# Optimization experiments

Hardware: AMD Instinct MI355X
Metric: run time of the kernel (lower is better)

## Reference

```python
import jax, jax.numpy as jnp
import numpy as np

B, T, E, H = 64, 256, 300, 512        # batch, longest_sequence, embed dim, hidden
V, NTAGS, NCLS, DFF = 50000, 17, 18, 256  # vocab, universal POS tags, output classes, dense hidden


def setup_inputs() -> dict:
    key = jax.random.key(0)
    ks = jax.random.split(key, 11)
    su = 1.0 / np.sqrt(H)  # PyTorch LSTMCell/Linear uniform init scale
    return {
        "tokens": jax.random.randint(ks[0], (B, T), 0, V),
        "tags": jax.random.randint(ks[1], (T,), 0, NTAGS),
        "emb": jax.random.normal(ks[2], (V, E), jnp.float32),
        "W_ih": jax.random.uniform(ks[3], (NTAGS, 4 * H, E), jnp.float32, -su, su),
        "W_hh": jax.random.uniform(ks[4], (NTAGS, 4 * H, H), jnp.float32, -su, su),
        "b_ih": jax.random.uniform(ks[5], (NTAGS, 4 * H), jnp.float32, -su, su),
        "b_hh": jax.random.uniform(ks[6], (NTAGS, 4 * H), jnp.float32, -su, su),
        "W1": jax.random.uniform(ks[7], (DFF, H), jnp.float32, -su, su),
        "b1": jax.random.uniform(ks[8], (DFF,), jnp.float32, -su, su),
        "W2": jax.random.uniform(ks[9], (NCLS, DFF), jnp.float32, -1.0 / np.sqrt(DFF), 1.0 / np.sqrt(DFF)),
        "b2": jax.random.uniform(ks[10], (NCLS,), jnp.float32, -1.0 / np.sqrt(DFF), 1.0 / np.sqrt(DFF)),
    }


def reference(tokens, tags, emb, W_ih, W_hh, b_ih, b_hh, W1, b1, W2, b2):
    x = emb[tokens]                     # [B, T, E] embedding lookup
    xs = jnp.swapaxes(x, 0, 1)          # [T, B, E] time-major for scan

    def step(carry, inp):
        h, c = carry
        xt, tag = inp                   # xt: [B, E], tag: scalar int routing the cell
        gates = (xt @ W_ih[tag].T + h @ W_hh[tag].T
                 + b_ih[tag] + b_hh[tag])            # [B, 4H]
        i, f, g, o = jnp.split(gates, 4, axis=-1)    # PyTorch LSTMCell gate order
        i = jax.nn.sigmoid(i)
        f = jax.nn.sigmoid(f)
        g = jnp.tanh(g)
        o = jax.nn.sigmoid(o)
        c = f * c + i * g
        h = o * jnp.tanh(c)
        return (h, c), None

    h0 = jnp.zeros((x.shape[0], H), x.dtype)
    (h, _), _ = jax.lax.scan(step, (h0, h0), (xs, tags))
    # dense head: Linear -> ReLU -> (Dropout inactive at eval) -> Linear
    hid = jax.nn.relu(h @ W1.T + b1)
    return hid @ W2.T + b2              # [B, NCLS] multiclass logits
```

## Files before the change

kernel.cpp:

```cpp
#include <hip/hip_runtime.h>
#include <cstdint>
#include <cstddef>

#define BB   64
#define TT   256
#define EE   300
#define HH   512
#define G4H  2048
#define NCLS 18
#define DFF  256
#define NBLK 256

__device__ __forceinline__ float fast_exp2(float x) { return __builtin_amdgcn_exp2f(x); }
__device__ __forceinline__ float sigmoid_f(float x) {
  return 1.0f / (1.0f + fast_exp2(x * -1.442695040888963f));
}
__device__ __forceinline__ float tanh_f(float x) {
  return 2.0f / (1.0f + fast_exp2(x * -2.885390081777927f)) - 1.0f;
}

__global__ __launch_bounds__(256) void xproj_kernel(
    const int* __restrict__ tokens, const int* __restrict__ tags,
    const float* __restrict__ emb, const float* __restrict__ W_ih,
    const float* __restrict__ b_ih, const float* __restrict__ b_hh,
    float* __restrict__ xW, int t0)
{
  const int tid  = threadIdx.x;
  const int lane = tid & 63;
  const int w    = tid >> 6;
  const int rs   = blockIdx.x & 127;
  const int tl   = blockIdx.x >> 7;
  const int t    = t0 + tl;
  const int tag  = tags[t];
  const int row0 = rs * 16;
  const int kbeg = __builtin_amdgcn_readfirstlane(w * 76);
  const bool full = (w != 3);

  const int tok = tokens[lane * TT + t];
  const float* xrow = emb + (size_t)tok * EE + kbeg;
  float xr[76];
  #pragma unroll
  for (int i = 0; i < 18; ++i) {
    const float4 v = *reinterpret_cast<const float4*>(xrow + i * 4);
    xr[i*4+0] = v.x; xr[i*4+1] = v.y; xr[i*4+2] = v.z; xr[i*4+3] = v.w;
  }
  if (full) {
    const float4 v = *reinterpret_cast<const float4*>(xrow + 72);
    xr[72] = v.x; xr[73] = v.y; xr[74] = v.z; xr[75] = v.w;
  } else {
    xr[72] = 0.f; xr[73] = 0.f; xr[74] = 0.f; xr[75] = 0.f;
  }

  const float* Wbase = W_ih + (size_t)tag * ((size_t)G4H * EE);
  __shared__ float red[4][16][64];
  #pragma unroll
  for (int r = 0; r < 16; ++r) {
    const float* Wr = Wbase + (size_t)(row0 + r) * EE + kbeg;
    float a = 0.f;
    #pragma unroll
    for (int k = 0; k < 72; ++k) a = fmaf(Wr[k], xr[k], a);
    if (full) {
      #pragma unroll
      for (int k = 72; k < 76; ++k) a = fmaf(Wr[k], xr[k], a);
    }
    red[w][r][lane] = a;
  }
  __syncthreads();
  #pragma unroll
  for (int it = 0; it < 4; ++it) {
    const int item = tid + it * 256;
    const int r = item >> 6, b = item & 63;
    const int row = row0 + r;
    float s = red[0][r][b] + red[1][r][b] + red[2][r][b] + red[3][r][b];
    s += b_ih[tag * G4H + row] + b_hh[tag * G4H + row];
    xW[((size_t)tl * G4H + row) * BB + b] = s;
  }
}

__global__ __launch_bounds__(1024) void lstm_seq_kernel(
    const int* __restrict__ tags, const float* __restrict__ W_hh,
    const float* __restrict__ xW, float* __restrict__ hA,
    float* __restrict__ hB, float* __restrict__ cst,
    float* __restrict__ hF, unsigned int* __restrict__ flags,
    int t0, int nsteps)
{
  const int tid  = threadIdx.x;
  const int lane = tid & 63;
  const int w    = tid >> 6;
  const int j0   = blockIdx.x * 2;
  const int kbeg = __builtin_amdgcn_readfirstlane(w * 32);

  __shared__ float red[16][8][64];
  __shared__ float gate[8][64];
  __shared__ float wbuf[2][8][512];

  const int ejj = tid >> 6, eb = tid & 63;
  const size_t eidx = (size_t)(j0 + ejj) * BB + eb;
  float creg = (tid < 128) ? cst[eidx] : 0.f;

  const int rr = tid >> 6, rb = tid & 63;
  const int rrow = j0 + (rr & 1) + (rr >> 1) * HH;
  float xw_cur = 0.f;
  if (tid < 512) xw_cur = xW[((size_t)0 * G4H + rrow) * BB + rb];

  const int pr  = w >> 1;
  const int phb = w & 1;
  const size_t prow_off = (size_t)(j0 + (pr & 1) + (pr >> 1) * HH) * HH
                          + phb * 256 + lane * 4;

  {
    const int tag0 = tags[t0];
    const float4 w0 = *reinterpret_cast<const float4*>(
        W_hh + (size_t)tag0 * ((size_t)G4H * HH) + prow_off);
    *reinterpret_cast<float4*>(&wbuf[0][pr][phb * 256 + lane * 4]) = w0;
  }
  __syncthreads();

  for (int s = 0; s < nsteps; ++s) {
    const int t   = t0 + s;
    const int cur = s & 1;
    const float* h_in  = (t & 1) ? hB : hA;
    float*       h_out = (t & 1) ? hA : hB;

    float xr[32];
    const float* hp0 = h_in + (size_t)kbeg * BB + lane;
    const float* hp1 = hp0 + 16 * BB;
    asm volatile(
      "global_load_dword %0,  %32, off sc0 sc1\n\t"
      "global_load_dword %1,  %32, off offset:256 sc0 sc1\n\t"
      "global_load_dword %2,  %32, off offset:512 sc0 sc1\n\t"
      "global_load_dword %3,  %32, off offset:768 sc0 sc1\n\t"
      "global_load_dword %4,  %32, off offset:1024 sc0 sc1\n\t"
      "global_load_dword %5,  %32, off offset:1280 sc0 sc1\n\t"
      "global_load_dword %6,  %32, off offset:1536 sc0 sc1\n\t"
      "global_load_dword %7,  %32, off offset:1792 sc0 sc1\n\t"
      "global_load_dword %8,  %32, off offset:2048 sc0 sc1\n\t"
      "global_load_dword %9,  %32, off offset:2304 sc0 sc1\n\t"
      "global_load_dword %10, %32, off offset:2560 sc0 sc1\n\t"
      "global_load_dword %11, %32, off offset:2816 sc0 sc1\n\t"
      "global_load_dword %12, %32, off offset:3072 sc0 sc1\n\t"
      "global_load_dword %13, %32, off offset:3328 sc0 sc1\n\t"
      "global_load_dword %14, %32, off offset:3584 sc0 sc1\n\t"
      "global_load_dword %15, %32, off offset:3840 sc0 sc1\n\t"
      "global_load_dword %16, %33, off sc0 sc1\n\t"
      "global_load_dword %17, %33, off offset:256 sc0 sc1\n\t"
      "global_load_dword %18, %33, off offset:512 sc0 sc1\n\t"
      "global_load_dword %19, %33, off offset:768 sc0 sc1\n\t"
      "global_load_dword %20, %33, off offset:1024 sc0 sc1\n\t"
      "global_load_dword %21, %33, off offset:1280 sc0 sc1\n\t"
      "global_load_dword %22, %33, off offset:1536 sc0 sc1\n\t"
      "global_load_dword %23, %33, off offset:1792 sc0 sc1\n\t"
      "global_load_dword %24, %33, off offset:2048 sc0 sc1\n\t"
      "global_load_dword %25, %33, off offset:2304 sc0 sc1\n\t"
      "global_load_dword %26, %33, off offset:2560 sc0 sc1\n\t"
      "global_load_dword %27, %33, off offset:2816 sc0 sc1\n\t"
      "global_load_dword %28, %33, off offset:3072 sc0 sc1\n\t"
      "global_load_dword %29, %33, off offset:3328 sc0 sc1\n\t"
      "global_load_dword %30, %33, off offset:3584 sc0 sc1\n\t"
      "global_load_dword %31, %33, off offset:3840 sc0 sc1\n\t"
      "s_waitcnt vmcnt(0)"
      : "=&v"(xr[0]),  "=&v"(xr[1]),  "=&v"(xr[2]),  "=&v"(xr[3]),
        "=&v"(xr[4]),  "=&v"(xr[5]),  "=&v"(xr[6]),  "=&v"(xr[7]),
        "=&v"(xr[8]),  "=&v"(xr[9]),  "=&v"(xr[10]), "=&v"(xr[11]),
        "=&v"(xr[12]), "=&v"(xr[13]), "=&v"(xr[14]), "=&v"(xr[15]),
        "=&v"(xr[16]), "=&v"(xr[17]), "=&v"(xr[18]), "=&v"(xr[19]),
        "=&v"(xr[20]), "=&v"(xr[21]), "=&v"(xr[22]), "=&v"(xr[23]),
        "=&v"(xr[24]), "=&v"(xr[25]), "=&v"(xr[26]), "=&v"(xr[27]),
        "=&v"(xr[28]), "=&v"(xr[29]), "=&v"(xr[30]), "=&v"(xr[31])
      : "v"(hp0), "v"(hp1)
      : "memory");

    const bool pre = (s + 1 < nsteps);
    float4 wpre;
    if (pre) {
      const int ntag = tags[t + 1];
      wpre = *reinterpret_cast<const float4*>(
          W_hh + (size_t)ntag * ((size_t)G4H * HH) + prow_off);
    }

    #pragma unroll
    for (int g = 0; g < 4; ++g) {
      #pragma unroll
      for (int jj = 0; jj < 2; ++jj) {
        const int r = g * 2 + jj;
        const float* Wr = &wbuf[cur][r][kbeg];
        float a = 0.f;
        #pragma unroll
        for (int i = 0; i < 8; ++i) {
          const float4 wv = *reinterpret_cast<const float4*>(Wr + i * 4);
          a = fmaf(wv.x, xr[i*4+0], a);
          a = fmaf(wv.y, xr[i*4+1], a);
          a = fmaf(wv.z, xr[i*4+2], a);
          a = fmaf(wv.w, xr[i*4+3], a);
        }
        red[w][r][lane] = a;
      }
    }

    if (pre) {
      *reinterpret_cast<float4*>(&wbuf[cur ^ 1][pr][phb * 256 + lane * 4]) = wpre;
    }
    __syncthreads();

    if (tid < 512) {
      float sacc = 0.f;
      #pragma unroll
      for (int ww = 0; ww < 16; ++ww) sacc += red[ww][rr][rb];
      gate[rr][rb] = sacc + xw_cur;
    }
    __syncthreads();
    if (tid < 128) {
      const float i_ = sigmoid_f(gate[0 + ejj][eb]);
      const float f_ = sigmoid_f(gate[2 + ejj][eb]);
      const float g_ = tanh_f   (gate[4 + ejj][eb]);
      const float o_ = sigmoid_f(gate[6 + ejj][eb]);
      creg = f_ * creg + i_ * g_;
      const float hval = o_ * tanh_f(creg);
      __hip_atomic_store(&h_out[eidx], hval, __ATOMIC_RELAXED,
                         __HIP_MEMORY_SCOPE_AGENT);
      if (t == TT - 1) hF[eidx] = hval;
    }
    __syncthreads();
    if (s != nsteps - 1) {
      if (tid == 0) {
        __hip_atomic_store(&flags[blockIdx.x * 16], (unsigned int)(s + 1),
                           __ATOMIC_RELAXED, __HIP_MEMORY_SCOPE_AGENT);
      }
      if (tid < 512) xw_cur = xW[((size_t)(s + 1) * G4H + rrow) * BB + rb];
      if (w == 0) {
        const unsigned int target = (unsigned int)(s + 1);
        for (;;) {
          const unsigned int f0 = __hip_atomic_load(&flags[(lane      ) * 16],
                                    __ATOMIC_RELAXED, __HIP_MEMORY_SCOPE_AGENT);
          const unsigned int f1 = __hip_atomic_load(&flags[(lane +  64) * 16],
                                    __ATOMIC_RELAXED, __HIP_MEMORY_SCOPE_AGENT);
          const unsigned int f2 = __hip_atomic_load(&flags[(lane + 128) * 16],
                                    __ATOMIC_RELAXED, __HIP_MEMORY_SCOPE_AGENT);
          const unsigned int f3 = __hip_atomic_load(&flags[(lane + 192) * 16],
                                    __ATOMIC_RELAXED, __HIP_MEMORY_SCOPE_AGENT);
          if (__all(f0 >= target && f1 >= target && f2 >= target && f3 >= target))
            break;
        }
      }
      __syncthreads();
    }
  }
  if (tid < 128) cst[eidx] = creg;
}

__global__ __launch_bounds__(1024) void head1_kernel(
    const float* __restrict__ W1, const float* __restrict__ b1,
    const float* __restrict__ hfin, float* __restrict__ hid)
{
  const int tid  = threadIdx.x;
  const int lane = tid & 63;
  const int w    = tid >> 6;
  const int row0 = blockIdx.x * 8;
  const int kbeg = __builtin_amdgcn_readfirstlane(w * 32);
  float xr[32];
  const float* hp = hfin + (size_t)kbeg * BB + lane;
  #pragma unroll
  for (int i = 0; i < 32; ++i) xr[i] = hp[i * BB];
  __shared__ float red[16][8][64];
  #pragma unroll
  for (int r = 0; r < 8; ++r) {
    const float* Wr = W1 + (size_t)(row0 + r) * HH + kbeg;
    float a = 0.f;
    #pragma unroll
    for (int k = 0; k < 32; ++k) a = fmaf(Wr[k], xr[k], a);
    red[w][r][lane] = a;
  }
  __syncthreads();
  if (tid < 512) {
    const int r = tid >> 6, b = tid & 63;
    float s = 0.f;
    #pragma unroll
    for (int ww = 0; ww < 16; ++ww) s += red[ww][r][b];
    s += b1[row0 + r];
    hid[(size_t)(row0 + r) * BB + b] = fmaxf(s, 0.f);
  }
}

__global__ __launch_bounds__(256) void head2_kernel(
    const float* __restrict__ W2, const float* __restrict__ b2,
    const float* __restrict__ hid, float* __restrict__ out)
{
  const int tid  = threadIdx.x;
  const int lane = tid & 63;
  const int w    = tid >> 6;
  const int kbeg = __builtin_amdgcn_readfirstlane(w * 64);
  float xr[64];
  const float* hp = hid + (size_t)kbeg * BB + lane;
  #pragma unroll
  for (int i = 0; i < 64; ++i) xr[i] = hp[i * BB];
  __shared__ float red[4][NCLS][64];
  #pragma unroll
  for (int r = 0; r < NCLS; ++r) {
    const float* Wr = W2 + (size_t)r * DFF + kbeg;
    float a = 0.f;
    #pragma unroll
    for (int k = 0; k < 64; ++k) a = fmaf(Wr[k], xr[k], a);
    red[w][r][lane] = a;
  }
  __syncthreads();
  for (int it = 0; it < 5; ++it) {
    const int item = tid + it * 256;
    if (item < NCLS * 64) {
      const int r = item >> 6, b = item & 63;
      float s = red[0][r][b] + red[1][r][b] + red[2][r][b] + red[3][r][b];
      out[(size_t)b * NCLS + r] = s + b2[r];
    }
  }
}

extern "C" void kernel_launch(void* const* d_in, const int* in_sizes, int n_in,
                              void* d_out, int out_size, void* d_ws, size_t ws_size,
                              hipStream_t stream)
{
  const int*   tokens = (const int*)  d_in[0];
  const int*   tags   = (const int*)  d_in[1];
  const float* emb    = (const float*)d_in[2];
  const float* W_ih   = (const float*)d_in[3];
  const float* W_hh   = (const float*)d_in[4];
  const float* b_ih   = (const float*)d_in[5];
  const float* b_hh   = (const float*)d_in[6];
  const float* W1     = (const float*)d_in[7];
  const float* b1     = (const float*)d_in[8];
  const float* W2     = (const float*)d_in[9];
  const float* b2     = (const float*)d_in[10];
  float* out = (float*)d_out;

  const size_t per_t = (size_t)G4H * BB * sizeof(float);
  int TCH = 8;
  for (int c = 256; c >= 8; c >>= 1) {
    if ((size_t)c * per_t + (4u << 20) <= ws_size) { TCH = c; break; }
  }
  char* p = (char*)d_ws;
  float* xW  = (float*)p;  p += (size_t)TCH * per_t;
  float* hA  = (float*)p;  p += (size_t)HH * BB * sizeof(float);
  float* hB  = (float*)p;  p += (size_t)HH * BB * sizeof(float);
  float* cst = (float*)p;  p += (size_t)HH * BB * sizeof(float);
  float* hF  = (float*)p;  p += (size_t)HH * BB * sizeof(float);
  float* hid = (float*)p;  p += (size_t)DFF * BB * sizeof(float);
  unsigned int* flags = (unsigned int*)p;

  (void)hipMemsetAsync(hA,  0, (size_t)HH * BB * sizeof(float), stream);
  (void)hipMemsetAsync(cst, 0, (size_t)HH * BB * sizeof(float), stream);

  for (int c0 = 0; c0 < TT; c0 += TCH) {
    xproj_kernel<<<dim3((unsigned)TCH * 128), dim3(256), 0, stream>>>(
        tokens, tags, emb, W_ih, b_ih, b_hh, xW, c0);
    (void)hipMemsetAsync(flags, 0, NBLK * 16 * sizeof(unsigned int), stream);
    {
      int t0 = c0, nsteps = TCH;
      void* args[] = { (void*)&tags, (void*)&W_hh, (void*)&xW,
                       (void*)&hA, (void*)&hB, (void*)&cst, (void*)&hF,
                       (void*)&flags, (void*)&t0, (void*)&nsteps };
      hipLaunchCooperativeKernel((const void*)lstm_seq_kernel,
                                 dim3(NBLK), dim3(1024), args, 0, stream);
    }
  }
  head1_kernel<<<dim3(32), dim3(1024), 0, stream>>>(W1, b1, hF, hid);
  head2_kernel<<<dim3(1), dim3(256), 0, stream>>>(W2, b2, hid, out);
}
```

Measured before the change: 1.864 ms.

## Fold gate reduction and cell update into one wave, poll flags per wave

Wave 0 of each block now does the whole cross-wave gate reduction, the activations and the h/c update for both hidden units. This replaces the earlier multi-wave reduction, which needed two extra __syncthreads per step. The reduction buffer is double-buffered by step parity so other waves can run ahead. Each wave now polls the 256 block flags itself at the start of the step (16 flags per wave), instead of wave 0 polling all flags and then a block barrier. This removes barriers from the serial recurrence critical path, at the cost of putting all elementwise work on one wave and adding more spin-load traffic on the flags.

Result: slower. 2.057 ms (+10.3%).

```diff
diff --git a/kernel.cpp b/kernel.cpp
--- a/kernel.cpp
+++ b/kernel.cpp
@@ -90,24 +90,25 @@
   const int j0   = blockIdx.x * 2;
   const int kbeg = __builtin_amdgcn_readfirstlane(w * 32);
 
-  __shared__ float red[16][8][64];
-  __shared__ float gate[8][64];
+  __shared__ float red[2][16][8][64];
   __shared__ float wbuf[2][8][512];
 
-  const int ejj = tid >> 6, eb = tid & 63;
-  const size_t eidx = (size_t)(j0 + ejj) * BB + eb;
-  float creg = (tid < 128) ? cst[eidx] : 0.f;
-
-  const int rr = tid >> 6, rb = tid & 63;
-  const int rrow = j0 + (rr & 1) + (rr >> 1) * HH;
-  float xw_cur = 0.f;
-  if (tid < 512) xw_cur = xW[((size_t)0 * G4H + rrow) * BB + rb];
+  float creg[2] = {0.f, 0.f};
+  float xw_cur[8];
+  if (w == 0) {
+    creg[0] = cst[(size_t)(j0 + 0) * BB + lane];
+    creg[1] = cst[(size_t)(j0 + 1) * BB + lane];
+    #pragma unroll
+    for (int r = 0; r < 8; ++r) {
+      const int row = j0 + (r & 1) + (r >> 1) * HH;
+      xw_cur[r] = xW[((size_t)0 * G4H + row) * BB + lane];
+    }
+  }
 
   const int pr  = w >> 1;
   const int phb = w & 1;
   const size_t prow_off = (size_t)(j0 + (pr & 1) + (pr >> 1) * HH) * HH
                           + phb * 256 + lane * 4;
-
   {
     const int tag0 = tags[t0];
     const float4 w0 = *reinterpret_cast<const float4*>(
@@ -116,11 +117,22 @@
   }
   __syncthreads();
 
+  const int pidx = 16 * w + (lane & 15);
+
   for (int s = 0; s < nsteps; ++s) {
     const int t   = t0 + s;
     const int cur = s & 1;
     const float* h_in  = (t & 1) ? hB : hA;
     float*       h_out = (t & 1) ? hA : hB;
+
+    if (s > 0) {
+      const unsigned int tgt = (unsigned int)s;
+      for (;;) {
+        const unsigned int f = __hip_atomic_load(&flags[pidx * 16],
+                                 __ATOMIC_RELAXED, __HIP_MEMORY_SCOPE_AGENT);
+        if (__all(f >= tgt)) break;
+      }
+    }
 
     float xr[32];
     const float* hp0 = h_in + (size_t)kbeg * BB + lane;
@@ -193,7 +205,7 @@
           a = fmaf(wv.z, xr[i*4+2], a);
           a = fmaf(wv.w, xr[i*4+3], a);
         }
-        red[w][r][lane] = a;
+        red[cur][w][r][lane] = a;
       }
     }
 
@@ -202,50 +214,53 @@
     }
     __syncthreads();
 
-    if (tid < 512) {
-      float sacc = 0.f;
+    if (w == 0) {
+      float g4[2][4];
       #pragma unroll
-      for (int ww = 0; ww < 16; ++ww) sacc += red[ww][rr][rb];
-      gate[rr][rb] = sacc + xw_cur;
-    }
-    __syncthreads();
-    if (tid < 128) {
-      const float i_ = sigmoid_f(gate[0 + ejj][eb]);
-      const float f_ = sigmoid_f(gate[2 + ejj][eb]);
-      const float g_ = tanh_f   (gate[4 + ejj][eb]);
-      const float o_ = sigmoid_f(gate[6 + ejj][eb]);
-      creg = f_ * creg + i_ * g_;
-      const float hval = o_ * tanh_f(creg);
-      __hip_atomic_store(&h_out[eidx], hval, __ATOMIC_RELAXED,
-                         __HIP_MEMORY_SCOPE_AGENT);
-      if (t == TT - 1) hF[eidx] = hval;
-    }
-    __syncthreads();
-    if (s != nsteps - 1) {
-      if (tid == 0) {
-        __hip_atomic_store(&flags[blockIdx.x * 16], (unsigned int)(s + 1),
+      for (int jj = 0; jj < 2; ++jj) {
+        #pragma unroll
+        for (int g = 0; g < 4; ++g) {
+          const int r = g * 2 + jj;
+          float sacc = xw_cur[r];
+          #pragma unroll
+          for (int ww = 0; ww < 16; ++ww) sacc += red[cur][ww][r][lane];
+          g4[jj][g] = sacc;
+        }
+      }
+      float hv[2];
+      #pragma unroll
+      for (int jj = 0; jj < 2; ++jj) {
+        const float i_ = sigmoid_f(g4[jj][0]);
+        const float f_ = sigmoid_f(g4[jj][1]);
+        const float gg = tanh_f   (g4[jj][2]);
+        const float o_ = sigmoid_f(g4[jj][3]);
+        creg[jj] = f_ * creg[jj] + i_ * gg;
+        hv[jj] = o_ * tanh_f(creg[jj]);
+        __hip_atomic_store(&h_out[(size_t)(j0 + jj) * BB + lane], hv[jj],
                            __ATOMIC_RELAXED, __HIP_MEMORY_SCOPE_AGENT);
       }
-      if (tid < 512) xw_cur = xW[((size_t)(s + 1) * G4H + rrow) * BB + rb];
-      if (w == 0) {
-        const unsigned int target = (unsigned int)(s + 1);
-        for (;;) {
-          const unsigned int f0 = __hip_atomic_load(&flags[(lane      ) * 16],
-                                    __ATOMIC_RELAXED, __HIP_MEMORY_SCOPE_AGENT);
-          const unsigned int f1 = __hip_atomic_load(&flags[(lane +  64) * 16],
-                                    __ATOMIC_RELAXED, __HIP_MEMORY_SCOPE_AGENT);
-          const unsigned int f2 = __hip_atomic_load(&flags[(lane + 128) * 16],
-                                    __ATOMIC_RELAXED, __HIP_MEMORY_SCOPE_AGENT);
-          const unsigned int f3 = __hip_atomic_load(&flags[(lane + 192) * 16],
-                                    __ATOMIC_RELAXED, __HIP_MEMORY_SCOPE_AGENT);
-          if (__all(f0 >= target && f1 >= target && f2 >= target && f3 >= target))
-            break;
+      if (t == TT - 1) {
+        hF[(size_t)(j0 + 0) * BB + lane] = hv[0];
+        hF[(size_t)(j0 + 1) * BB + lane] = hv[1];
+      }
+      if (s != nsteps - 1) {
+        asm volatile("s_waitcnt vmcnt(0)" ::: "memory");
+        if (lane == 0) {
+          __hip_atomic_store(&flags[blockIdx.x * 16], (unsigned int)(s + 1),
+                             __ATOMIC_RELAXED, __HIP_MEMORY_SCOPE_AGENT);
         }
-      }
-      __syncthreads();
-    }
-  }
-  if (tid < 128) cst[eidx] = creg;
+        #pragma unroll
+        for (int r = 0; r < 8; ++r) {
+          const int row = j0 + (r & 1) + (r >> 1) * HH;
+          xw_cur[r] = xW[((size_t)(s + 1) * G4H + row) * BB + lane];
+        }
+      }
+    }
+  }
+  if (w == 0) {
+    cst[(size_t)(j0 + 0) * BB + lane] = creg[0];
+    cst[(size_t)(j0 + 1) * BB + lane] = creg[1];
+  }
 }
 
 __global__ __launch_bounds__(1024) void head1_kernel(
```
